# Kernel optimization log

Measured on AMD Instinct MI355X. Metric: run time of the kernel, lower is better.

Reference implementation:

```python
import jax, jax.numpy as jnp
import numpy as np

N = 1_000_000
F_IN = 3
GRID = 480
B = 2
EPS = 1e-5


def setup_inputs() -> dict:
    key = jax.random.key(0)
    ks = jax.random.split(key, 24)
    pt_fea = jax.random.normal(ks[0], (N, F_IN), dtype=jnp.float32)
    xy_ind = jax.random.randint(ks[1], (N, 2), 0, GRID, dtype=jnp.int64)

    # batch-id prepended (F.pad(xy_ind,(1,0),value=i_batch)), then unique rows.
    batch_id = np.arange(N, dtype=np.int64) // (N // B)
    ind_np = np.asarray(xy_ind)
    lin = batch_id * (GRID * GRID) + ind_np[:, 0] * GRID + ind_np[:, 1]
    unq_lin, unq_inv = np.unique(lin, return_inverse=True)  # sorted == lexsorted rows
    unq = np.stack([unq_lin // (GRID * GRID), (unq_lin // GRID) % GRID, unq_lin % GRID], axis=1)

    def lin_w(k, fin, fout):
        return 0.05 * jax.random.normal(k, (fin, fout), dtype=jnp.float32)

    dims = [F_IN, 64, 128, 256, 128]
    params = {}
    # BN affine params: bn0 on input, bn1..bn3 after linears 1..3
    for i, d in enumerate([F_IN, 64, 128, 256]):
        params[f"bn{i}_g"] = jnp.ones((d,), jnp.float32)
        params[f"bn{i}_b"] = jnp.zeros((d,), jnp.float32)
    for i in range(4):
        params[f"W{i+1}"] = lin_w(ks[2 + i], dims[i], dims[i + 1])
        params[f"b{i+1}"] = jnp.zeros((dims[i + 1],), jnp.float32)

    return dict(pt_fea=pt_fea, xy_ind=xy_ind,
                unq=jnp.asarray(unq, jnp.int64), unq_inv=jnp.asarray(unq_inv, jnp.int32),
                **params)


def _bn(x, g, b):
    # training-mode BatchNorm1d: batch stats, biased variance
    m = jnp.mean(x, axis=0)
    v = jnp.var(x, axis=0)
    return (x - m) * jax.lax.rsqrt(v + EPS) * g + b


def reference(pt_fea, xy_ind, unq, unq_inv,
              bn0_g, bn0_b, bn1_g, bn1_b, bn2_g, bn2_b, bn3_g, bn3_b,
              W1, b1, W2, b2, W3, b3, W4, b4):
    h = _bn(pt_fea, bn0_g, bn0_b)
    h = jax.nn.relu(_bn(h @ W1 + b1, bn1_g, bn1_b))
    h = jax.nn.relu(_bn(h @ W2 + b2, bn2_g, bn2_b))
    h = jax.nn.relu(_bn(h @ W3 + b3, bn3_g, bn3_b))
    h = h @ W4 + b4  # [N, 128]
    pooled = jax.ops.segment_max(h, unq_inv, num_segments=unq.shape[0])  # [U, 128]
    return unq, pooled
```

## Files before the change

### kernel.cpp

```cpp
#include <hip/hip_runtime.h>
#include <math.h>

typedef unsigned int u32;
typedef unsigned short u16;

#define EPS 1e-5f
#define PTS 64

#define S0 0
#define Q0 16
#define S1 32
#define Q1 96
#define S2 160
#define Q2 288
#define S3 416
#define Q3 672

#define Z4S 132

typedef __attribute__((ext_vector_type(8))) short v8s;
typedef __attribute__((ext_vector_type(4))) float v4f;
typedef __attribute__((ext_vector_type(2))) unsigned int v2u;

#define MFMA(a,b,c) __builtin_amdgcn_mfma_f32_16x16x32_bf16(a,b,c,0,0,0)

#define W2H 0
#define W2L 8192
#define W3H 16384
#define W3L 49152
#define W4H 81920
#define W4L 114688
__device__ __align__(16) u16 g_wfrag[147456];

__device__ float g_acc[1024];
__device__ float g_st[1024];
__device__ int   g_is64;
__device__ int   g_inv64;
__device__ int   g_umax;
__device__ long  g_U;

__device__ __forceinline__ float bf2f(u16 b){ return __uint_as_float(((u32)b) << 16); }
__device__ __forceinline__ u16 f2bf(float f){
  u32 u = __float_as_uint(f);
  return (u16)((u + 0x7fffu + ((u >> 16) & 1u)) >> 16);
}

__device__ __forceinline__ u32 encf(float f){
  u32 u = __float_as_uint(f);
  return (u & 0x80000000u) ? ~u : (u | 0x80000000u);
}
__device__ __forceinline__ float decf(u32 u){
  return __uint_as_float((u & 0x80000000u) ? (u ^ 0x80000000u) : ~u);
}
#define ENC_NEG_INF 0x007FFFFFu

__device__ __forceinline__ void waveRedArr(float* v, int n){
  #pragma unroll
  for (int off = 32; off > 0; off >>= 1)
    for (int i = 0; i < n; ++i) v[i] += __shfl_xor(v[i], off, 64);
}

template<int FIN, int FOUT>
__device__ __forceinline__ void chunk16(const u16* hsrc, int lane,
    const float* __restrict__ W, const float* __restrict__ bias,
    int j0, float acc[16])
{
  const int j0u = __builtin_amdgcn_readfirstlane(j0);
  #pragma unroll
  for (int jj = 0; jj < 16; ++jj) acc[jj] = bias[j0u + jj];
  #pragma unroll 4
  for (int k = 0; k < FIN; ++k){
    const float hk = bf2f(hsrc[k*PTS + lane]);
    const float* Wr = W + (long)k*FOUT + j0u;
    #pragma unroll
    for (int jj = 0; jj < 16; ++jj) acc[jj] = fmaf(hk, Wr[jj], acc[jj]);
  }
}

template<int FIN, int FOUT>
__device__ __forceinline__ void chunk16_acc(const u16* hsrc, int lane,
    const float* __restrict__ W, int j0, int k0, float acc[16])
{
  const int j0u = __builtin_amdgcn_readfirstlane(j0);
  #pragma unroll 4
  for (int k = 0; k < FIN; ++k){
    const float hk = bf2f(hsrc[k*PTS + lane]);
    const float* Wr = W + (long)(k0 + k)*FOUT + j0u;
    #pragma unroll
    for (int jj = 0; jj < 16; ++jj) acc[jj] = fmaf(hk, Wr[jj], acc[jj]);
  }
}

__device__ __forceinline__ void emitStats(float acc[16], bool valid, int lane, int j0,
                                          float* bs, float* bq){
  #pragma unroll
  for (int jj = 0; jj < 16; ++jj){
    float v = valid ? acc[jj] : 0.f;
    float sq[2] = {v, v*v};
    waveRedArr(sq, 2);
    if (lane == 0){ atomicAdd(&bs[j0+jj], sq[0]); atomicAdd(&bq[j0+jj], sq[1]); }
  }
}
__device__ __forceinline__ void emitH(float acc[16], int lane, int j0u, int soff, int qoff, u16* hdst){
  #pragma unroll
  for (int jj = 0; jj < 16; ++jj){
    float z = fmaxf(acc[jj]*g_st[soff+j0u+jj] + g_st[qoff+j0u+jj], 0.f);
    hdst[(j0u+jj)*PTS + lane] = f2bf(z);
  }
}

__global__ void kreset(){
  if (threadIdx.x == 0) g_umax = 0;
  for (int i = threadIdx.x; i < 1024; i += blockDim.x) g_acc[i] = 0.f;
}

__global__ void ksniff_inv(const u32* __restrict__ w, long nwords){
  __shared__ int any;
  if (threadIdx.x == 0) any = 0;
  __syncthreads();
  for (long i = 2L*threadIdx.x + 1; i < nwords; i += 2L*blockDim.x){
    if (w[i] != 0u){ any = 1; break; }
  }
  __syncthreads();
  if (threadIdx.x == 0) g_inv64 = (any == 0) ? 1 : 0;
}

__global__ __launch_bounds__(256) void ksegU(const void* __restrict__ invv, int N){
  const int inv64 = g_inv64;
  int m = 0;
  const int stride = gridDim.x*blockDim.x;
  if (inv64){
    const long long* q = (const long long*)invv;
    for (int i = blockIdx.x*blockDim.x + threadIdx.x; i < N; i += stride)
      m = max(m, (int)q[i]);
  } else {
    const int* q = (const int*)invv;
    for (int i = blockIdx.x*blockDim.x + threadIdx.x; i < N; i += stride)
      m = max(m, q[i]);
  }
  #pragma unroll
  for (int off = 32; off > 0; off >>= 1) m = max(m, __shfl_xor(m, off, 64));
  if ((threadIdx.x & 63) == 0) atomicMax(&g_umax, m);
}

__global__ void ksniff_unq(const u32* __restrict__ w){
  __shared__ int any;
  if (threadIdx.x == 0){ g_U = (long)g_umax + 1; any = 0; }
  __syncthreads();
  const long nwords = 3L*g_U;
  for (long i = 2L*threadIdx.x + 1; i < nwords; i += 2L*blockDim.x){
    if (w[i] != 0u){ any = 1; break; }
  }
  __syncthreads();
  if (threadIdx.x == 0) g_is64 = (any == 0) ? 1 : 0;
}

__global__ void kpoolinit(u32* __restrict__ outu, long outSize){
  const long U = g_U;
  const long lo = 3*U;
  const long hi = (131*U < outSize) ? 131*U : outSize;
  const long i0 = (long)blockIdx.x*blockDim.x + threadIdx.x;
  const long stride = (long)gridDim.x*blockDim.x;
  for (long i = lo + i0; i < hi; i += stride) outu[i] = ENC_NEG_INF;
}

__global__ void kdecode(u32* __restrict__ outu, long outSize){
  const long U = g_U;
  const long lo = 3*U;
  const long hi = (131*U < outSize) ? 131*U : outSize;
  const long i0 = (long)blockIdx.x*blockDim.x + threadIdx.x;
  const long stride = (long)gridDim.x*blockDim.x;
  for (long i = lo + i0; i < hi; i += stride)
    outu[i] = __float_as_uint(decf(outu[i]));
}

__global__ void kunq(float* __restrict__ out, const void* __restrict__ unqv, long outSize){
  const long U = g_U;
  const long n = (3*U < outSize) ? 3*U : outSize;
  const long i0 = (long)blockIdx.x*blockDim.x + threadIdx.x;
  const long stride = (long)gridDim.x*blockDim.x;
  if (g_is64){
    const long long* uq = (const long long*)unqv;
    for (long i = i0; i < n; i += stride) out[i] = (float)uq[i];
  } else {
    const int* uq = (const int*)unqv;
    for (long i = i0; i < n; i += stride) out[i] = (float)uq[i];
  }
}

__global__ __launch_bounds__(256) void kstats0(const float* __restrict__ x, int N){
  __shared__ float red[4][9];
  float a[9];
  #pragma unroll
  for (int i = 0; i < 9; ++i) a[i] = 0.f;
  const int stride = gridDim.x*blockDim.x;
  for (int p = blockIdx.x*blockDim.x + threadIdx.x; p < N; p += stride){
    float v0 = x[(size_t)p*3 + 0], v1 = x[(size_t)p*3 + 1], v2 = x[(size_t)p*3 + 2];
    a[0]+=v0; a[1]+=v1; a[2]+=v2;
    a[3]+=v0*v0; a[4]+=v1*v1; a[5]+=v2*v2;
    a[6]+=v0*v1; a[7]+=v0*v2; a[8]+=v1*v2;
  }
  waveRedArr(a, 9);
  const int w = threadIdx.x >> 6, lane = threadIdx.x & 63;
  if (lane == 0){
    #pragma unroll
    for (int i = 0; i < 9; ++i) red[w][i] = a[i];
  }
  __syncthreads();
  if (threadIdx.x < 9){
    float t = 0.f;
    #pragma unroll
    for (int k = 0; k < 4; ++k) t += red[k][threadIdx.x];
    const int c = threadIdx.x;
    atomicAdd(&g_acc[(c < 3) ? (S0 + c) : (Q0 + (c - 3))], t);
  }
}

__global__ void kfin(int dim, int soff, int qoff,
                     const float* __restrict__ g, const float* __restrict__ b, float invN){
  const int j = threadIdx.x;
  if (j >= dim) return;
  const float m = g_acc[soff+j]*invN;
  const float var = fmaxf(g_acc[qoff+j]*invN - m*m, 0.f);
  const float s = g[j]*rsqrtf(var + EPS);
  g_st[soff+j] = s;
  g_st[qoff+j] = b[j] - m*s;
}

__global__ void kfin1(const float* __restrict__ g1, const float* __restrict__ b1bn,
                      const float* __restrict__ W1, const float* __restrict__ b1lin,
                      float invN){
  const int j = threadIdx.x;
  if (j >= 64) return;
  float m0[3], s0[3], t0[3];
  #pragma unroll
  for (int c = 0; c < 3; ++c){
    m0[c] = g_acc[S0+c]*invN;
    s0[c] = g_st[S0+c];
    t0[c] = g_st[Q0+c];
  }
  float C[3][3];
  C[0][0] = g_acc[Q0+0]*invN - m0[0]*m0[0];
  C[1][1] = g_acc[Q0+1]*invN - m0[1]*m0[1];
  C[2][2] = g_acc[Q0+2]*invN - m0[2]*m0[2];
  C[0][1] = C[1][0] = g_acc[Q0+3]*invN - m0[0]*m0[1];
  C[0][2] = C[2][0] = g_acc[Q0+4]*invN - m0[0]*m0[2];
  C[1][2] = C[2][1] = g_acc[Q0+5]*invN - m0[1]*m0[2];

  float wj[3] = {W1[0*64 + j], W1[1*64 + j], W1[2*64 + j]};
  float mean = b1lin[j];
  #pragma unroll
  for (int c = 0; c < 3; ++c) mean += (m0[c]*s0[c] + t0[c])*wj[c];
  float var = 0.f;
  #pragma unroll
  for (int a = 0; a < 3; ++a)
    #pragma unroll
    for (int b = 0; b < 3; ++b)
      var += wj[a]*s0[a]*wj[b]*s0[b]*C[a][b];
  var = fmaxf(var, 0.f);
  const float sc = g1[j]*rsqrtf(var + EPS);
  g_st[S1+j] = sc;
  g_st[Q1+j] = b1bn[j] - mean*sc;
}


__global__ void kprep(const float* __restrict__ W2, const float* __restrict__ W3,
                      const float* __restrict__ W4){
  int t = blockIdx.x*blockDim.x + threadIdx.x;
  int frag = t >> 6, lane = t & 63;
  if (frag >= 144) return;
  const float* W; int F, fb, kb; u16 *hi, *lo;
  if (frag < 16){
    fb = frag >> 1; kb = frag & 1; W = W2; F = 128;
    size_t o = (size_t)((fb*2 + kb)*64 + lane)*8;
    hi = g_wfrag + W2H + o; lo = g_wfrag + W2L + o;
  } else if (frag < 80){
    int f = frag - 16; fb = f >> 2; kb = f & 3; W = W3; F = 256;
    size_t o = (size_t)((fb*4 + kb)*64 + lane)*8;
    hi = g_wfrag + W3H + o; lo = g_wfrag + W3L + o;
  } else {
    int f = frag - 80; fb = f >> 3; kb = f & 7; W = W4; F = 128;
    size_t o = (size_t)((fb*8 + kb)*64 + lane)*8;
    hi = g_wfrag + W4H + o; lo = g_wfrag + W4L + o;
  }
  const int feat = fb*16 + (lane & 15);
  const int k0 = kb*32 + (lane >> 4)*8;
  #pragma unroll
  for (int jj = 0; jj < 8; ++jj){
    float wv = W[(size_t)(k0 + jj)*F + feat];
    u16 h = f2bf(wv);
    hi[jj] = h;
    lo[jj] = f2bf(wv - bf2f(h));
  }
}

__global__ __launch_bounds__(256) void kpass2m(
    const float* __restrict__ x,
    const float* __restrict__ W1, const float* __restrict__ b1,
    const float* __restrict__ b2, u16* __restrict__ z2ws, int N)
{
  __shared__ __align__(16) u16 h1f[4096];
  __shared__ __align__(16) u16 z2f[8192];
  const int tid = threadIdx.x, w = tid >> 6, lane = tid & 63;
  const int g = lane >> 4, p15 = lane & 15;

  float s2[2][4], q2[2][4];
  #pragma unroll
  for (int f = 0; f < 2; ++f)
    #pragma unroll
    for (int r = 0; r < 4; ++r){ s2[f][r] = 0.f; q2[f][r] = 0.f; }

  const int j0u = __builtin_amdgcn_readfirstlane(w*16);
  const int nb = (N + 63) >> 6;
  for (int b = blockIdx.x; b < nb; b += gridDim.x){
    const int p = b*64 + lane;
    const bool valid = p < N;
    {
      float h0[3];
      #pragma unroll
      for (int c = 0; c < 3; ++c){
        float xv = valid ? x[(size_t)p*3 + c] : 0.f;
        h0[c] = xv*g_st[S0 + c] + g_st[Q0 + c];
      }
      float acc[16];
      #pragma unroll
      for (int jj = 0; jj < 16; ++jj) acc[jj] = b1[j0u + jj];
      #pragma unroll
      for (int k = 0; k < 3; ++k){
        const float* Wr = W1 + k*64 + j0u;
        #pragma unroll
        for (int jj = 0; jj < 16; ++jj) acc[jj] = fmaf(h0[k], Wr[jj], acc[jj]);
      }
      u16 hb[16];
      #pragma unroll
      for (int jj = 0; jj < 16; ++jj)
        hb[jj] = f2bf(fmaxf(acc[jj]*g_st[S1+j0u+jj] + g_st[Q1+j0u+jj], 0.f));
      const int kb = w >> 1;
      const int lA = ((2*w) & 3)*16 + p15;
      union { v8s v; u32 u[4]; } pa, pbk;
      #pragma unroll
      for (int q = 0; q < 4; ++q){
        pa.u[q]  = (u32)hb[2*q]     | ((u32)hb[2*q+1] << 16);
        pbk.u[q] = (u32)hb[8+2*q]   | ((u32)hb[8+2*q+1] << 16);
      }
      *(v8s*)(h1f + ((kb*4 + g)*64 + lA     )*8) = pa.v;
      *(v8s*)(h1f + ((kb*4 + g)*64 + lA + 16)*8) = pbk.v;
    }
    __syncthreads();
    #pragma unroll
    for (int f = 0; f < 2; ++f){
      const int fb = w*2 + f;
      const v4f bias = *(const v4f*)(b2 + fb*16 + g*4);
      v4f acc[4];
      #pragma unroll
      for (int pb = 0; pb < 4; ++pb) acc[pb] = bias;
      #pragma unroll
      for (int kb = 0; kb < 2; ++kb){
        const v8s Ah = *(const v8s*)(g_wfrag + W2H + (size_t)((fb*2+kb)*64 + lane)*8);
        const v8s Al = *(const v8s*)(g_wfrag + W2L + (size_t)((fb*2+kb)*64 + lane)*8);
        #pragma unroll
        for (int pb = 0; pb < 4; ++pb){
          const v8s B = *(const v8s*)(h1f + ((kb*4 + pb)*64 + lane)*8);
          acc[pb] = MFMA(Ah, B, acc[pb]);
          acc[pb] = MFMA(Al, B, acc[pb]);
        }
      }
      #pragma unroll
      for (int pb = 0; pb < 4; ++pb){
        const bool pv = (b*64 + pb*16 + p15) < N;
        u16 zb[4];
        #pragma unroll
        for (int r = 0; r < 4; ++r){
          float v = pv ? acc[pb][r] : 0.f;
          s2[f][r] += v; q2[f][r] += v*v;
          zb[r] = f2bf(acc[pb][r]);
        }
        const int kb2 = fb >> 1;
        const int lp = ((2*fb + (g >> 1)) & 3)*16 + p15;
        v2u dv; dv[0] = (u32)zb[0] | ((u32)zb[1] << 16);
        dv[1] = (u32)zb[2] | ((u32)zb[3] << 16);
        *(v2u*)(z2f + ((kb2*4 + pb)*64 + lp)*8 + 4*(g & 1)) = dv;
      }
    }
    __syncthreads();
    {
      u16* dst = z2ws + (size_t)b*8192;
      #pragma unroll
      for (int i = 0; i < 4; ++i){
        const int idx = (i*256 + tid)*8;
        *(v8s*)(dst + idx) = *(const v8s*)(z2f + idx);
      }
    }
    __syncthreads();
  }
  #pragma unroll
  for (int f = 0; f < 2; ++f)
    #pragma unroll
    for (int r = 0; r < 4; ++r){
      float s = s2[f][r], q = q2[f][r];
      #pragma unroll
      for (int off = 1; off < 16; off <<= 1){
        s += __shfl_xor(s, off, 64); q += __shfl_xor(q, off, 64);
      }
      if (p15 == 0){
        const int feat = (w*2 + f)*16 + g*4 + r;
        atomicAdd(&g_acc[S2 + feat], s);
        atomicAdd(&g_acc[Q2 + feat], q);
      }
    }
}

__global__ __launch_bounds__(256) void kpass3m(
    const u16* __restrict__ z2ws, const float* __restrict__ b3,
    u16* __restrict__ z3ws, int N)
{
  __shared__ __align__(16) u16 h2f[8192];
  __shared__ __align__(16) u16 z3f[16384];
  const int tid = threadIdx.x, w = tid >> 6, lane = tid & 63;
  const int g = lane >> 4, p15 = lane & 15;

  const int k0 = w*32 + g*8;
  const v4f sA = *(const v4f*)(g_st + S2 + k0);
  const v4f sB = *(const v4f*)(g_st + S2 + k0 + 4);
  const v4f tA = *(const v4f*)(g_st + Q2 + k0);
  const v4f tB = *(const v4f*)(g_st + Q2 + k0 + 4);

  float s3[4][4], q3[4][4];
  #pragma unroll
  for (int i = 0; i < 4; ++i)
    #pragma unroll
    for (int r = 0; r < 4; ++r){ s3[i][r] = 0.f; q3[i][r] = 0.f; }

  const int nb = (N + 63) >> 6;
  for (int b = blockIdx.x; b < nb; b += gridDim.x){
    #pragma unroll
    for (int pb = 0; pb < 4; ++pb){
      union { v8s v; u32 u[4]; } in, outv;
      in.v = *(const v8s*)(z2ws + (size_t)b*8192 + ((w*4 + pb)*64 + lane)*8);
      #pragma unroll
      for (int q = 0; q < 4; ++q){
        const int e = q*2;
        float z0 = bf2f((u16)(in.u[q] & 0xFFFFu));
        float z1 = bf2f((u16)(in.u[q] >> 16));
        const float sc0 = (e   < 4) ? sA[e]   : sB[e-4];
        const float sh0 = (e   < 4) ? tA[e]   : tB[e-4];
        const float sc1 = (e+1 < 4) ? sA[e+1] : sB[e-3];
        const float sh1 = (e+1 < 4) ? tA[e+1] : tB[e-3];
        z0 = fmaxf(fmaf(z0, sc0, sh0), 0.f);
        z1 = fmaxf(fmaf(z1, sc1, sh1), 0.f);
        outv.u[q] = (u32)f2bf(z0) | ((u32)f2bf(z1) << 16);
      }
      *(v8s*)(h2f + ((w*4 + pb)*64 + lane)*8) = outv.v;
    }
    __syncthreads();
    #pragma unroll
    for (int i = 0; i < 4; ++i){
      const int fb = w*4 + i;
      const v4f bias = *(const v4f*)(b3 + fb*16 + g*4);
      v4f acc[4];
      #pragma unroll
      for (int pb = 0; pb < 4; ++pb) acc[pb] = bias;
      #pragma unroll
      for (int kb = 0; kb < 4; ++kb){
        const v8s Ah = *(const v8s*)(g_wfrag + W3H + (size_t)((fb*4+kb)*64 + lane)*8);
        const v8s Al = *(const v8s*)(g_wfrag + W3L + (size_t)((fb*4+kb)*64 + lane)*8);
        #pragma unroll
        for (int pb = 0; pb < 4; ++pb){
          const v8s B = *(const v8s*)(h2f + ((kb*4 + pb)*64 + lane)*8);
          acc[pb] = MFMA(Ah, B, acc[pb]);
          acc[pb] = MFMA(Al, B, acc[pb]);
        }
      }
      #pragma unroll
      for (int pb = 0; pb < 4; ++pb){
        const bool pv = (b*64 + pb*16 + p15) < N;
        u16 zb[4];
        #pragma unroll
        for (int r = 0; r < 4; ++r){
          float v = pv ? acc[pb][r] : 0.f;
          s3[i][r] += v; q3[i][r] += v*v;
          zb[r] = f2bf(acc[pb][r]);
        }
        const int kb3 = fb >> 1;
        const int lp = ((2*fb + (g >> 1)) & 3)*16 + p15;
        v2u dv; dv[0] = (u32)zb[0] | ((u32)zb[1] << 16);
        dv[1] = (u32)zb[2] | ((u32)zb[3] << 16);
        *(v2u*)(z3f + ((kb3*4 + pb)*64 + lp)*8 + 4*(g & 1)) = dv;
      }
    }
    __syncthreads();
    {
      u16* dst = z3ws + (size_t)b*16384;
      #pragma unroll
      for (int i2 = 0; i2 < 8; ++i2){
        const int idx = (i2*256 + tid)*8;
        *(v8s*)(dst + idx) = *(const v8s*)(z3f + idx);
      }
    }
    __syncthreads();
  }
  #pragma unroll
  for (int i = 0; i < 4; ++i)
    #pragma unroll
    for (int r = 0; r < 4; ++r){
      float s = s3[i][r], q = q3[i][r];
      #pragma unroll
      for (int off = 1; off < 16; off <<= 1){
        s += __shfl_xor(s, off, 64); q += __shfl_xor(q, off, 64);
      }
      if (p15 == 0){
        const int feat = (w*4 + i)*16 + g*4 + r;
        atomicAdd(&g_acc[S3 + feat], s);
        atomicAdd(&g_acc[Q3 + feat], q);
      }
    }
}

__global__ __launch_bounds__(256) void kpass4m(
    const void* __restrict__ unq_inv_v, const float* __restrict__ b4,
    const u16* __restrict__ z3ws, u32* __restrict__ outu, int N, long outSize)
{
  __shared__ __align__(16) u16 buf[16896];
  __shared__ int seg_s[64];
  u16* const h3f = buf;
  float* const z4 = (float*)buf;

  const long U = g_U;
  const int inv64 = g_inv64;
  const long loEl = 3*U;
  const long hiEl = (131*U < outSize) ? 131*U : outSize;
  const int tid = threadIdx.x, w = tid >> 6, lane = tid & 63;
  const int g = lane >> 4, p15 = lane & 15;

  const int k0a = w*64 + g*8;
  const v4f sA0 = *(const v4f*)(g_st + S3 + k0a);
  const v4f sA1 = *(const v4f*)(g_st + S3 + k0a + 4);
  const v4f tA0 = *(const v4f*)(g_st + Q3 + k0a);
  const v4f tA1 = *(const v4f*)(g_st + Q3 + k0a + 4);
  const v4f sB0 = *(const v4f*)(g_st + S3 + k0a + 32);
  const v4f sB1 = *(const v4f*)(g_st + S3 + k0a + 36);
  const v4f tB0 = *(const v4f*)(g_st + Q3 + k0a + 32);
  const v4f tB1 = *(const v4f*)(g_st + Q3 + k0a + 36);

  const int nb = (N + 63) >> 6;
  for (int b = blockIdx.x; b < nb; b += gridDim.x){
    const int p = b*64 + lane;
    const bool valid = p < N;

    #pragma unroll
    for (int kk = 0; kk < 2; ++kk){
      const int kb3 = 2*w + kk;
      #pragma unroll
      for (int pb = 0; pb < 4; ++pb){
        union { v8s v; u32 u[4]; } in, outv;
        in.v = *(const v8s*)(z3ws + (size_t)b*16384 + ((kb3*4 + pb)*64 + lane)*8);
        #pragma unroll
        for (int q = 0; q < 4; ++q){
          const int e = q*2;
          float z0 = bf2f((u16)(in.u[q] & 0xFFFFu));
          float z1 = bf2f((u16)(in.u[q] >> 16));
          const float sc0 = kk ? ((e   < 4) ? sB0[e]   : sB1[e-4]) : ((e   < 4) ? sA0[e]   : sA1[e-4]);
          const float sh0 = kk ? ((e   < 4) ? tB0[e]   : tB1[e-4]) : ((e   < 4) ? tA0[e]   : tA1[e-4]);
          const float sc1 = kk ? ((e+1 < 4) ? sB0[e+1] : sB1[e-3]) : ((e+1 < 4) ? sA0[e+1] : sA1[e-3]);
          const float sh1 = kk ? ((e+1 < 4) ? tB0[e+1] : tB1[e-3]) : ((e+1 < 4) ? tA0[e+1] : tA1[e-3]);
          z0 = fmaxf(fmaf(z0, sc0, sh0), 0.f);
          z1 = fmaxf(fmaf(z1, sc1, sh1), 0.f);
          outv.u[q] = (u32)f2bf(z0) | ((u32)f2bf(z1) << 16);
        }
        *(v8s*)(h3f + ((kb3*4 + pb)*64 + lane)*8) = outv.v;
      }
    }
    if (w == 0){
      int sg = -1;
      if (valid){
        long s = inv64 ? (long)((const long long*)unq_inv_v)[p]
                       : (long)((const int*)unq_inv_v)[p];
        sg = (int)s;
      }
      seg_s[lane] = (sg >= 0 && sg < U &&
                     loEl + (long)sg*128 + 128 <= hiEl) ? sg : -1;
    }
    __syncthreads();

    v4f acc[2][4];
    #pragma unroll
    for (int f = 0; f < 2; ++f){
      const int fb = w*2 + f;
      const v4f bias = *(const v4f*)(b4 + fb*16 + g*4);
      #pragma unroll
      for (int pb = 0; pb < 4; ++pb) acc[f][pb] = bias;
      #pragma unroll
      for (int kb = 0; kb < 8; ++kb){
        const v8s Ah = *(const v8s*)(g_wfrag + W4H + (size_t)((fb*8+kb)*64 + lane)*8);
        const v8s Al = *(const v8s*)(g_wfrag + W4L + (size_t)((fb*8+kb)*64 + lane)*8);
        #pragma unroll
        for (int pb = 0; pb < 4; ++pb){
          const v8s B = *(const v8s*)(h3f + ((kb*4 + pb)*64 + lane)*8);
          acc[f][pb] = MFMA(Ah, B, acc[f][pb]);
          acc[f][pb] = MFMA(Al, B, acc[f][pb]);
        }
      }
    }
    __syncthreads();
    #pragma unroll
    for (int f = 0; f < 2; ++f){
      const int fb = w*2 + f;
      #pragma unroll
      for (int pb = 0; pb < 4; ++pb)
        *(v4f*)(z4 + (pb*16 + p15)*Z4S + fb*16 + g*4) = acc[f][pb];
    }
    __syncthreads();
    #pragma unroll 4
    for (int pt2 = 0; pt2 < 64; pt2 += 2){
      const int pt = pt2 + (tid >> 7);
      const int fI = tid & 127;
      const int sg = seg_s[pt];
      if (sg >= 0)
        atomicMax(outu + loEl + (long)sg*128 + fI, encf(z4[pt*Z4S + fI]));
    }
    __syncthreads();
  }
}

extern "C" void kernel_launch(void* const* d_in, const int* in_sizes, int n_in,
                              void* d_out, int out_size, void* d_ws, size_t ws_size,
                              hipStream_t stream)
{
  const float* x       = (const float*)d_in[0];
  const void*  unq     = d_in[2];
  const void*  unq_inv = d_in[3];
  const float* bn_g[4] = {(const float*)d_in[4], (const float*)d_in[6], (const float*)d_in[8], (const float*)d_in[10]};
  const float* bn_b[4] = {(const float*)d_in[5], (const float*)d_in[7], (const float*)d_in[9], (const float*)d_in[11]};
  const float* W1 = (const float*)d_in[12]; const float* b1 = (const float*)d_in[13];
  const float* W2 = (const float*)d_in[14]; const float* b2 = (const float*)d_in[15];
  const float* W3 = (const float*)d_in[16]; const float* b3 = (const float*)d_in[17];
  const float* W4 = (const float*)d_in[18]; const float* b4 = (const float*)d_in[19];

  const int N = in_sizes[0] / 3;
  float* out = (float*)d_out;
  u32* outu = (u32*)d_out;
  const float invN = 1.0f / (float)N;
  const long outSize = (long)out_size;

  const size_t nb64 = (size_t)((N + 63) / 64);
  u16* z3ws = (u16*)d_ws;
  u16* z2ws = z3ws + nb64*16384;

  kreset<<<1, 1024, 0, stream>>>();
  ksniff_inv<<<1, 1024, 0, stream>>>((const u32*)unq_inv, (long)N);
  ksegU<<<512, 256, 0, stream>>>(unq_inv, N);
  ksniff_unq<<<1, 1024, 0, stream>>>((const u32*)unq);
  kpoolinit<<<2048, 256, 0, stream>>>(outu, outSize);

  kstats0<<<1024, 256, 0, stream>>>(x, N);
  kfin<<<1, 256, 0, stream>>>(3, S0, Q0, bn_g[0], bn_b[0], invN);
  kfin1<<<1, 64, 0, stream>>>(bn_g[1], bn_b[1], W1, b1, invN);

  kprep<<<36, 256, 0, stream>>>(W2, W3, W4);
  kpass2m<<<2048, 256, 0, stream>>>(x, W1, b1, b2, z2ws, N);
  kfin<<<1, 256, 0, stream>>>(128, S2, Q2, bn_g[2], bn_b[2], invN);
  kpass3m<<<1536, 256, 0, stream>>>(z2ws, b3, z3ws, N);
  kfin<<<1, 256, 0, stream>>>(256, S3, Q3, bn_g[3], bn_b[3], invN);
  kpass4m<<<1024, 256, 0, stream>>>(unq_inv, b4, z3ws, outu, N, outSize);

  kdecode<<<2048, 256, 0, stream>>>(outu, outSize);
  kunq<<<2048, 256, 0, stream>>>(out, unq, outSize);
}
```

Before: 1.744 ms.

## Recompute earlier MLP layers per pass instead of storing bf16 intermediates

Drops the z2/z3 workspace round-trips through global memory. Each later pass now recomputes layers 1–2 (and layer 3 in the final pass) from the raw input using MFMA. This trades extra matrix compute for removing large intermediate writes and reads, about 16 KB and 32 KB per 64-point block. The decode and unq kernels are also merged into one finishing kernel, and the final pass uses more shared memory and a smaller grid.

```diff
diff --git a/kernel.cpp b/kernel.cpp
--- a/kernel.cpp
+++ b/kernel.cpp
@@ -5,7 +5,6 @@
 typedef unsigned short u16;
 
 #define EPS 1e-5f
-#define PTS 64
 
 #define S0 0
 #define Q0 16
@@ -58,55 +57,6 @@
   #pragma unroll
   for (int off = 32; off > 0; off >>= 1)
     for (int i = 0; i < n; ++i) v[i] += __shfl_xor(v[i], off, 64);
-}
-
-template<int FIN, int FOUT>
-__device__ __forceinline__ void chunk16(const u16* hsrc, int lane,
-    const float* __restrict__ W, const float* __restrict__ bias,
-    int j0, float acc[16])
-{
-  const int j0u = __builtin_amdgcn_readfirstlane(j0);
-  #pragma unroll
-  for (int jj = 0; jj < 16; ++jj) acc[jj] = bias[j0u + jj];
-  #pragma unroll 4
-  for (int k = 0; k < FIN; ++k){
-    const float hk = bf2f(hsrc[k*PTS + lane]);
-    const float* Wr = W + (long)k*FOUT + j0u;
-    #pragma unroll
-    for (int jj = 0; jj < 16; ++jj) acc[jj] = fmaf(hk, Wr[jj], acc[jj]);
-  }
-}
-
-template<int FIN, int FOUT>
-__device__ __forceinline__ void chunk16_acc(const u16* hsrc, int lane,
-    const float* __restrict__ W, int j0, int k0, float acc[16])
-{
-  const int j0u = __builtin_amdgcn_readfirstlane(j0);
-  #pragma unroll 4
-  for (int k = 0; k < FIN; ++k){
-    const float hk = bf2f(hsrc[k*PTS + lane]);
-    const float* Wr = W + (long)(k0 + k)*FOUT + j0u;
-    #pragma unroll
-    for (int jj = 0; jj < 16; ++jj) acc[jj] = fmaf(hk, Wr[jj], acc[jj]);
-  }
-}
-
-__device__ __forceinline__ void emitStats(float acc[16], bool valid, int lane, int j0,
-                                          float* bs, float* bq){
-  #pragma unroll
-  for (int jj = 0; jj < 16; ++jj){
-    float v = valid ? acc[jj] : 0.f;
-    float sq[2] = {v, v*v};
-    waveRedArr(sq, 2);
-    if (lane == 0){ atomicAdd(&bs[j0+jj], sq[0]); atomicAdd(&bq[j0+jj], sq[1]); }
-  }
-}
-__device__ __forceinline__ void emitH(float acc[16], int lane, int j0u, int soff, int qoff, u16* hdst){
-  #pragma unroll
-  for (int jj = 0; jj < 16; ++jj){
-    float z = fmaxf(acc[jj]*g_st[soff+j0u+jj] + g_st[qoff+j0u+jj], 0.f);
-    hdst[(j0u+jj)*PTS + lane] = f2bf(z);
-  }
 }
 
 __global__ void kreset(){
@@ -164,28 +114,22 @@
   for (long i = lo + i0; i < hi; i += stride) outu[i] = ENC_NEG_INF;
 }
 
-__global__ void kdecode(u32* __restrict__ outu, long outSize){
+__global__ void kfinish(float* __restrict__ out, u32* __restrict__ outu,
+                        const void* __restrict__ unqv, long outSize){
   const long U = g_U;
-  const long lo = 3*U;
+  const long n3 = (3*U < outSize) ? 3*U : outSize;
   const long hi = (131*U < outSize) ? 131*U : outSize;
-  const long i0 = (long)blockIdx.x*blockDim.x + threadIdx.x;
-  const long stride = (long)gridDim.x*blockDim.x;
-  for (long i = lo + i0; i < hi; i += stride)
-    outu[i] = __float_as_uint(decf(outu[i]));
-}
-
-__global__ void kunq(float* __restrict__ out, const void* __restrict__ unqv, long outSize){
-  const long U = g_U;
-  const long n = (3*U < outSize) ? 3*U : outSize;
   const long i0 = (long)blockIdx.x*blockDim.x + threadIdx.x;
   const long stride = (long)gridDim.x*blockDim.x;
   if (g_is64){
     const long long* uq = (const long long*)unqv;
-    for (long i = i0; i < n; i += stride) out[i] = (float)uq[i];
+    for (long i = i0; i < n3; i += stride) out[i] = (float)uq[i];
   } else {
     const int* uq = (const int*)unqv;
-    for (long i = i0; i < n; i += stride) out[i] = (float)uq[i];
-  }
+    for (long i = i0; i < n3; i += stride) out[i] = (float)uq[i];
+  }
+  for (long i = n3 + i0; i < hi; i += stride)
+    outu[i] = __float_as_uint(decf(outu[i]));
 }
 
 __global__ __launch_bounds__(256) void kstats0(const float* __restrict__ x, int N){
@@ -294,15 +238,88 @@
   }
 }
 
-__global__ __launch_bounds__(256) void kpass2m(
+__device__ __forceinline__ void stageL1(const float* __restrict__ x,
+    const float* __restrict__ W1, const float* __restrict__ b1,
+    u16* h1f, int p, bool valid, int w, int lane, int j0u)
+{
+  const int g = lane >> 4, p15 = lane & 15;
+  float h0[3];
+  #pragma unroll
+  for (int c = 0; c < 3; ++c){
+    float xv = valid ? x[(size_t)p*3 + c] : 0.f;
+    h0[c] = xv*g_st[S0 + c] + g_st[Q0 + c];
+  }
+  float acc[16];
+  #pragma unroll
+  for (int jj = 0; jj < 16; ++jj) acc[jj] = b1[j0u + jj];
+  #pragma unroll
+  for (int k = 0; k < 3; ++k){
+    const float* Wr = W1 + k*64 + j0u;
+    #pragma unroll
+    for (int jj = 0; jj < 16; ++jj) acc[jj] = fmaf(h0[k], Wr[jj], acc[jj]);
+  }
+  u16 hb[16];
+  #pragma unroll
+  for (int jj = 0; jj < 16; ++jj)
+    hb[jj] = f2bf(fmaxf(acc[jj]*g_st[S1+j0u+jj] + g_st[Q1+j0u+jj], 0.f));
+  const int kb = w >> 1;
+  const int lA = ((2*w) & 3)*16 + p15;
+  union { v8s v; u32 u[4]; } pa, pbk;
+  #pragma unroll
+  for (int q = 0; q < 4; ++q){
+    pa.u[q]  = (u32)hb[2*q]   | ((u32)hb[2*q+1] << 16);
+    pbk.u[q] = (u32)hb[8+2*q] | ((u32)hb[8+2*q+1] << 16);
+  }
+  *(v8s*)(h1f + ((kb*4 + g)*64 + lA     )*8) = pa.v;
+  *(v8s*)(h1f + ((kb*4 + g)*64 + lA + 16)*8) = pbk.v;
+}
+
+__device__ __forceinline__ void gemmL2(const u16* h1f, const float* __restrict__ b2,
+    int fb, int g, int lane, v4f acc[4])
+{
+  const v4f bias = *(const v4f*)(b2 + fb*16 + g*4);
+  #pragma unroll
+  for (int pb = 0; pb < 4; ++pb) acc[pb] = bias;
+  #pragma unroll
+  for (int kb = 0; kb < 2; ++kb){
+    const v8s Ah = *(const v8s*)(g_wfrag + W2H + (size_t)((fb*2+kb)*64 + lane)*8);
+    const v8s Al = *(const v8s*)(g_wfrag + W2L + (size_t)((fb*2+kb)*64 + lane)*8);
+    #pragma unroll
+    for (int pb = 0; pb < 4; ++pb){
+      const v8s B = *(const v8s*)(h1f + ((kb*4 + pb)*64 + lane)*8);
+      acc[pb] = MFMA(Ah, B, acc[pb]);
+      acc[pb] = MFMA(Al, B, acc[pb]);
+    }
+  }
+}
+
+__device__ __forceinline__ void stageBF(u16* dst, const v4f acc[4],
+    const v4f sc, const v4f sh, int fb, int g, int p15)
+{
+  const int kbo = fb >> 1;
+  const int lp = ((2*fb + (g >> 1)) & 3)*16 + p15;
+  #pragma unroll
+  for (int pb = 0; pb < 4; ++pb){
+    u16 zb[4];
+    #pragma unroll
+    for (int r = 0; r < 4; ++r)
+      zb[r] = f2bf(fmaxf(fmaf(acc[pb][r], sc[r], sh[r]), 0.f));
+    v2u dv;
+    dv[0] = (u32)zb[0] | ((u32)zb[1] << 16);
+    dv[1] = (u32)zb[2] | ((u32)zb[3] << 16);
+    *(v2u*)(dst + ((kbo*4 + pb)*64 + lp)*8 + 4*(g & 1)) = dv;
+  }
+}
+
+__global__ __launch_bounds__(256) void kpassB(
     const float* __restrict__ x,
     const float* __restrict__ W1, const float* __restrict__ b1,
-    const float* __restrict__ b2, u16* __restrict__ z2ws, int N)
+    const float* __restrict__ b2, int N)
 {
   __shared__ __align__(16) u16 h1f[4096];
-  __shared__ __align__(16) u16 z2f[8192];
   const int tid = threadIdx.x, w = tid >> 6, lane = tid & 63;
   const int g = lane >> 4, p15 = lane & 15;
+  const int j0u = __builtin_amdgcn_readfirstlane(w*16);
 
   float s2[2][4], q2[2][4];
   #pragma unroll
@@ -310,85 +327,23 @@
     #pragma unroll
     for (int r = 0; r < 4; ++r){ s2[f][r] = 0.f; q2[f][r] = 0.f; }
 
-  const int j0u = __builtin_amdgcn_readfirstlane(w*16);
   const int nb = (N + 63) >> 6;
   for (int b = blockIdx.x; b < nb; b += gridDim.x){
     const int p = b*64 + lane;
-    const bool valid = p < N;
-    {
-      float h0[3];
-      #pragma unroll
-      for (int c = 0; c < 3; ++c){
-        float xv = valid ? x[(size_t)p*3 + c] : 0.f;
-        h0[c] = xv*g_st[S0 + c] + g_st[Q0 + c];
-      }
-      float acc[16];
-      #pragma unroll
-      for (int jj = 0; jj < 16; ++jj) acc[jj] = b1[j0u + jj];
-      #pragma unroll
-      for (int k = 0; k < 3; ++k){
-        const float* Wr = W1 + k*64 + j0u;
-        #pragma unroll
-        for (int jj = 0; jj < 16; ++jj) acc[jj] = fmaf(h0[k], Wr[jj], acc[jj]);
-      }
-      u16 hb[16];
-      #pragma unroll
-      for (int jj = 0; jj < 16; ++jj)
-        hb[jj] = f2bf(fmaxf(acc[jj]*g_st[S1+j0u+jj] + g_st[Q1+j0u+jj], 0.f));
-      const int kb = w >> 1;
-      const int lA = ((2*w) & 3)*16 + p15;
-      union { v8s v; u32 u[4]; } pa, pbk;
-      #pragma unroll
-      for (int q = 0; q < 4; ++q){
-        pa.u[q]  = (u32)hb[2*q]     | ((u32)hb[2*q+1] << 16);
-        pbk.u[q] = (u32)hb[8+2*q]   | ((u32)hb[8+2*q+1] << 16);
-      }
-      *(v8s*)(h1f + ((kb*4 + g)*64 + lA     )*8) = pa.v;
-      *(v8s*)(h1f + ((kb*4 + g)*64 + lA + 16)*8) = pbk.v;
-    }
+    stageL1(x, W1, b1, h1f, p, p < N, w, lane, j0u);
     __syncthreads();
     #pragma unroll
     for (int f = 0; f < 2; ++f){
-      const int fb = w*2 + f;
-      const v4f bias = *(const v4f*)(b2 + fb*16 + g*4);
       v4f acc[4];
-      #pragma unroll
-      for (int pb = 0; pb < 4; ++pb) acc[pb] = bias;
-      #pragma unroll
-      for (int kb = 0; kb < 2; ++kb){
-        const v8s Ah = *(const v8s*)(g_wfrag + W2H + (size_t)((fb*2+kb)*64 + lane)*8);
-        const v8s Al = *(const v8s*)(g_wfrag + W2L + (size_t)((fb*2+kb)*64 + lane)*8);
-        #pragma unroll
-        for (int pb = 0; pb < 4; ++pb){
-          const v8s B = *(const v8s*)(h1f + ((kb*4 + pb)*64 + lane)*8);
-          acc[pb] = MFMA(Ah, B, acc[pb]);
-          acc[pb] = MFMA(Al, B, acc[pb]);
-        }
-      }
+      gemmL2(h1f, b2, w*2 + f, g, lane, acc);
       #pragma unroll
       for (int pb = 0; pb < 4; ++pb){
         const bool pv = (b*64 + pb*16 + p15) < N;
-        u16 zb[4];
         #pragma unroll
         for (int r = 0; r < 4; ++r){
           float v = pv ? acc[pb][r] : 0.f;
           s2[f][r] += v; q2[f][r] += v*v;
-          zb[r] = f2bf(acc[pb][r]);
         }
-        const int kb2 = fb >> 1;
-        const int lp = ((2*fb + (g >> 1)) & 3)*16 + p15;
-        v2u dv; dv[0] = (u32)zb[0] | ((u32)zb[1] << 16);
-        dv[1] = (u32)zb[2] | ((u32)zb[3] << 16);
-        *(v2u*)(z2f + ((kb2*4 + pb)*64 + lp)*8 + 4*(g & 1)) = dv;
-      }
-    }
-    __syncthreads();
-    {
-      u16* dst = z2ws + (size_t)b*8192;
-      #pragma unroll
-      for (int i = 0; i < 4; ++i){
-        const int idx = (i*256 + tid)*8;
-        *(v8s*)(dst + idx) = *(const v8s*)(z2f + idx);
       }
     }
     __syncthreads();
@@ -410,20 +365,24 @@
     }
 }
 
-__global__ __launch_bounds__(256) void kpass3m(
-    const u16* __restrict__ z2ws, const float* __restrict__ b3,
-    u16* __restrict__ z3ws, int N)
+__global__ __launch_bounds__(256) void kpassC(
+    const float* __restrict__ x,
+    const float* __restrict__ W1, const float* __restrict__ b1,
+    const float* __restrict__ b2, const float* __restrict__ b3, int N)
 {
-  __shared__ __align__(16) u16 h2f[8192];
-  __shared__ __align__(16) u16 z3f[16384];
+  __shared__ __align__(16) u16 buf[12288];
+  u16* const h2f = buf;
+  u16* const h1f = buf + 8192;
   const int tid = threadIdx.x, w = tid >> 6, lane = tid & 63;
   const int g = lane >> 4, p15 = lane & 15;
-
-  const int k0 = w*32 + g*8;
-  const v4f sA = *(const v4f*)(g_st + S2 + k0);
-  const v4f sB = *(const v4f*)(g_st + S2 + k0 + 4);
-  const v4f tA = *(const v4f*)(g_st + Q2 + k0);
-  const v4f tB = *(const v4f*)(g_st + Q2 + k0 + 4);
+  const int j0u = __builtin_amdgcn_readfirstlane(w*16);
+
+  v4f sc2[2], sh2[2];
+  #pragma unroll
+  for (int f = 0; f < 2; ++f){
+    sc2[f] = *(const v4f*)(g_st + S2 + (w*2+f)*16 + g*4);
+    sh2[f] = *(const v4f*)(g_st + Q2 + (w*2+f)*16 + g*4);
+  }
 
   float s3[4][4], q3[4][4];
   #pragma unroll
@@ -433,24 +392,14 @@
 
   const int nb = (N + 63) >> 6;
   for (int b = blockIdx.x; b < nb; b += gridDim.x){
-    #pragma unroll
-    for (int pb = 0; pb < 4; ++pb){
-      union { v8s v; u32 u[4]; } in, outv;
-      in.v = *(const v8s*)(z2ws + (size_t)b*8192 + ((w*4 + pb)*64 + lane)*8);
-      #pragma unroll
-      for (int q = 0; q < 4; ++q){
-        const int e = q*2;
-        float z0 = bf2f((u16)(in.u[q] & 0xFFFFu));
-        float z1 = bf2f((u16)(in.u[q] >> 16));
-        const float sc0 = (e   < 4) ? sA[e]   : sB[e-4];
-        const float sh0 = (e   < 4) ? tA[e]   : tB[e-4];
-        const float sc1 = (e+1 < 4) ? sA[e+1] : sB[e-3];
-        const float sh1 = (e+1 < 4) ? tA[e+1] : tB[e-3];
-        z0 = fmaxf(fmaf(z0, sc0, sh0), 0.f);
-        z1 = fmaxf(fmaf(z1, sc1, sh1), 0.f);
-        outv.u[q] = (u32)f2bf(z0) | ((u32)f2bf(z1) << 16);
-      }
-      *(v8s*)(h2f + ((w*4 + pb)*64 + lane)*8) = outv.v;
+    const int p = b*64 + lane;
+    stageL1(x, W1, b1, h1f, p, p < N, w, lane, j0u);
+    __syncthreads();
+    #pragma unroll
+    for (int f = 0; f < 2; ++f){
+      v4f acc[4];
+      gemmL2(h1f, b2, w*2 + f, g, lane, acc);
+      stageBF(h2f, acc, sc2[f], sh2[f], w*2 + f, g, p15);
     }
     __syncthreads();
     #pragma unroll
@@ -474,27 +423,11 @@
       #pragma unroll
       for (int pb = 0; pb < 4; ++pb){
         const bool pv = (b*64 + pb*16 + p15) < N;
-        u16 zb[4];
         #pragma unroll
         for (int r = 0; r < 4; ++r){
           float v = pv ? acc[pb][r] : 0.f;
           s3[i][r] += v; q3[i][r] += v*v;
-          zb[r] = f2bf(acc[pb][r]);
         }
-        const int kb3 = fb >> 1;
-        const int lp = ((2*fb + (g >> 1)) & 3)*16 + p15;
-        v2u dv; dv[0] = (u32)zb[0] | ((u32)zb[1] << 16);
-        dv[1] = (u32)zb[2] | ((u32)zb[3] << 16);
-        *(v2u*)(z3f + ((kb3*4 + pb)*64 + lp)*8 + 4*(g & 1)) = dv;
-      }
-    }
-    __syncthreads();
-    {
-      u16* dst = z3ws + (size_t)b*16384;
-      #pragma unroll
-      for (int i2 = 0; i2 < 8; ++i2){
-        const int idx = (i2*256 + tid)*8;
-        *(v8s*)(dst + idx) = *(const v8s*)(z3f + idx);
       }
     }
     __syncthreads();
@@ -516,13 +449,18 @@
     }
 }
 
-__global__ __launch_bounds__(256) void kpass4m(
-    const void* __restrict__ unq_inv_v, const float* __restrict__ b4,
-    const u16* __restrict__ z3ws, u32* __restrict__ outu, int N, long outSize)
+__global__ __launch_bounds__(256) void kpassD(
+    const float* __restrict__ x, const void* __restrict__ unq_inv_v,
+    const float* __restrict__ W1, const float* __restrict__ b1,
+    const float* __restrict__ b2, const float* __restrict__ b4,
+    const float* __restrict__ b3,
+    u32* __restrict__ outu, int N, long outSize)
 {
-  __shared__ __align__(16) u16 buf[16896];
+  __shared__ __align__(16) u16 buf[24576];
   __shared__ int seg_s[64];
-  u16* const h3f = buf;
+  u16* const h2f = buf;
+  u16* const h1f = buf + 8192;
+  u16* const h3f = buf + 8192;
   float* const z4 = (float*)buf;
 
   const long U = g_U;
@@ -531,45 +469,21 @@
   const long hiEl = (131*U < outSize) ? 131*U : outSize;
   const int tid = threadIdx.x, w = tid >> 6, lane = tid & 63;
   const int g = lane >> 4, p15 = lane & 15;
-
-  const int k0a = w*64 + g*8;
-  const v4f sA0 = *(const v4f*)(g_st + S3 + k0a);
-  const v4f sA1 = *(const v4f*)(g_st + S3 + k0a + 4);
-  const v4f tA0 = *(const v4f*)(g_st + Q3 + k0a);
-  const v4f tA1 = *(const v4f*)(g_st + Q3 + k0a + 4);
-  const v4f sB0 = *(const v4f*)(g_st + S3 + k0a + 32);
-  const v4f sB1 = *(const v4f*)(g_st + S3 + k0a + 36);
-  const v4f tB0 = *(const v4f*)(g_st + Q3 + k0a + 32);
-  const v4f tB1 = *(const v4f*)(g_st + Q3 + k0a + 36);
+  const int j0u = __builtin_amdgcn_readfirstlane(w*16);
+
+  v4f sc2[2], sh2[2];
+  #pragma unroll
+  for (int f = 0; f < 2; ++f){
+    sc2[f] = *(const v4f*)(g_st + S2 + (w*2+f)*16 + g*4);
+    sh2[f] = *(const v4f*)(g_st + Q2 + (w*2+f)*16 + g*4);
+  }
 
   const int nb = (N + 63) >> 6;
   for (int b = blockIdx.x; b < nb; b += gridDim.x){
     const int p = b*64 + lane;
     const bool valid = p < N;
 
-    #pragma unroll
-    for (int kk = 0; kk < 2; ++kk){
-      const int kb3 = 2*w + kk;
-      #pragma unroll
-      for (int pb = 0; pb < 4; ++pb){
-        union { v8s v; u32 u[4]; } in, outv;
-        in.v = *(const v8s*)(z3ws + (size_t)b*16384 + ((kb3*4 + pb)*64 + lane)*8);
-        #pragma unroll
-        for (int q = 0; q < 4; ++q){
-          const int e = q*2;
-          float z0 = bf2f((u16)(in.u[q] & 0xFFFFu));
-          float z1 = bf2f((u16)(in.u[q] >> 16));
-          const float sc0 = kk ? ((e   < 4) ? sB0[e]   : sB1[e-4]) : ((e   < 4) ? sA0[e]   : sA1[e-4]);
-          const float sh0 = kk ? ((e   < 4) ? tB0[e]   : tB1[e-4]) : ((e   < 4) ? tA0[e]   : tA1[e-4]);
-          const float sc1 = kk ? ((e+1 < 4) ? sB0[e+1] : sB1[e-3]) : ((e+1 < 4) ? sA0[e+1] : sA1[e-3]);
-          const float sh1 = kk ? ((e+1 < 4) ? tB0[e+1] : tB1[e-3]) : ((e+1 < 4) ? tA0[e+1] : tA1[e-3]);
-          z0 = fmaxf(fmaf(z0, sc0, sh0), 0.f);
-          z1 = fmaxf(fmaf(z1, sc1, sh1), 0.f);
-          outv.u[q] = (u32)f2bf(z0) | ((u32)f2bf(z1) << 16);
-        }
-        *(v8s*)(h3f + ((kb3*4 + pb)*64 + lane)*8) = outv.v;
-      }
-    }
+    stageL1(x, W1, b1, h1f, p, valid, w, lane, j0u);
     if (w == 0){
       int sg = -1;
       if (valid){
@@ -582,13 +496,45 @@
     }
     __syncthreads();
 
-    v4f acc[2][4];
+    #pragma unroll
+    for (int f = 0; f < 2; ++f){
+      v4f acc[4];
+      gemmL2(h1f, b2, w*2 + f, g, lane, acc);
+      stageBF(h2f, acc, sc2[f], sh2[f], w*2 + f, g, p15);
+    }
+    __syncthreads();
+
+    #pragma unroll
+    for (int i = 0; i < 4; ++i){
+      const int fb = w*4 + i;
+      const v4f bias = *(const v4f*)(b3 + fb*16 + g*4);
+      v4f acc[4];
+      #pragma unroll
+      for (int pb = 0; pb < 4; ++pb) acc[pb] = bias;
+      #pragma unroll
+      for (int kb = 0; kb < 4; ++kb){
+        const v8s Ah = *(const v8s*)(g_wfrag + W3H + (size_t)((fb*4+kb)*64 + lane)*8);
+        const v8s Al = *(const v8s*)(g_wfrag + W3L + (size_t)((fb*4+kb)*64 + lane)*8);
+        #pragma unroll
+        for (int pb = 0; pb < 4; ++pb){
+          const v8s B = *(const v8s*)(h2f + ((kb*4 + pb)*64 + lane)*8);
+          acc[pb] = MFMA(Ah, B, acc[pb]);
+          acc[pb] = MFMA(Al, B, acc[pb]);
+        }
+      }
+      const v4f sc3 = *(const v4f*)(g_st + S3 + fb*16 + g*4);
+      const v4f sh3 = *(const v4f*)(g_st + Q3 + fb*16 + g*4);
+      stageBF(h3f, acc, sc3, sh3, fb, g, p15);
+    }
+    __syncthreads();
+
+    v4f acc4[2][4];
     #pragma unroll
     for (int f = 0; f < 2; ++f){
       const int fb = w*2 + f;
       const v4f bias = *(const v4f*)(b4 + fb*16 + g*4);
       #pragma unroll
-      for (int pb = 0; pb < 4; ++pb) acc[f][pb] = bias;
+      for (int pb = 0; pb < 4; ++pb) acc4[f][pb] = bias;
       #pragma unroll
       for (int kb = 0; kb < 8; ++kb){
         const v8s Ah = *(const v8s*)(g_wfrag + W4H + (size_t)((fb*8+kb)*64 + lane)*8);
@@ -596,20 +542,22 @@
         #pragma unroll
         for (int pb = 0; pb < 4; ++pb){
           const v8s B = *(const v8s*)(h3f + ((kb*4 + pb)*64 + lane)*8);
-          acc[f][pb] = MFMA(Ah, B, acc[f][pb]);
-          acc[f][pb] = MFMA(Al, B, acc[f][pb]);
+          acc4[f][pb] = MFMA(Ah, B, acc4[f][pb]);
+          acc4[f][pb] = MFMA(Al, B, acc4[f][pb]);
         }
       }
     }
     __syncthreads();
+
     #pragma unroll
     for (int f = 0; f < 2; ++f){
       const int fb = w*2 + f;
       #pragma unroll
       for (int pb = 0; pb < 4; ++pb)
-        *(v4f*)(z4 + (pb*16 + p15)*Z4S + fb*16 + g*4) = acc[f][pb];
-    }
-    __syncthreads();
+        *(v4f*)(z4 + (pb*16 + p15)*Z4S + fb*16 + g*4) = acc4[f][pb];
+    }
+    __syncthreads();
+
     #pragma unroll 4
     for (int pt2 = 0; pt2 < 64; pt2 += 2){
       const int pt = pt2 + (tid >> 7);
@@ -642,10 +590,6 @@
   const float invN = 1.0f / (float)N;
   const long outSize = (long)out_size;
 
-  const size_t nb64 = (size_t)((N + 63) / 64);
-  u16* z3ws = (u16*)d_ws;
-  u16* z2ws = z3ws + nb64*16384;
-
   kreset<<<1, 1024, 0, stream>>>();
   ksniff_inv<<<1, 1024, 0, stream>>>((const u32*)unq_inv, (long)N);
   ksegU<<<512, 256, 0, stream>>>(unq_inv, N);
@@ -657,12 +601,11 @@
   kfin1<<<1, 64, 0, stream>>>(bn_g[1], bn_b[1], W1, b1, invN);
 
   kprep<<<36, 256, 0, stream>>>(W2, W3, W4);
-  kpass2m<<<2048, 256, 0, stream>>>(x, W1, b1, b2, z2ws, N);
+  kpassB<<<2048, 256, 0, stream>>>(x, W1, b1, b2, N);
   kfin<<<1, 256, 0, stream>>>(128, S2, Q2, bn_g[2], bn_b[2], invN);
-  kpass3m<<<1536, 256, 0, stream>>>(z2ws, b3, z3ws, N);
+  kpassC<<<1536, 256, 0, stream>>>(x, W1, b1, b2, b3, N);
   kfin<<<1, 256, 0, stream>>>(256, S3, Q3, bn_g[3], bn_b[3], invN);
-  kpass4m<<<1024, 256, 0, stream>>>(unq_inv, b4, z3ws, outu, N, outSize);
-
-  kdecode<<<2048, 256, 0, stream>>>(outu, outSize);
-  kunq<<<2048, 256, 0, stream>>>(out, unq, outSize);
-}
+  kpassD<<<768, 256, 0, stream>>>(x, unq_inv, W1, b1, b2, b4, b3, outu, N, outSize);
+
+  kfinish<<<2048, 256, 0, stream>>>(out, outu, unq, outSize);
+}
```

Measured after the change: 1.745 ms. About the same (+0.0%).
